# Performance work log

Measured on AMD Instinct MI355X. Metric: run time of the kernel, lower is better.

The kernel has to match this reference:

```python
import jax, jax.numpy as jnp
import numpy as np


def conv1x1(x, W, b):
    # 1x1 Conv2d == per-pixel linear over channels. x: [B,C,H,W], W: [O,C], b: [O]
    return jnp.einsum('oc,bchw->bohw', W, x) + b[None, :, None, None]


def setup_inputs() -> dict:
    key = jax.random.key(0)
    ks = jax.random.split(key, 18)
    B, C, Hd, H, W = 16, 64, 64, 32, 32
    s = 0.05
    f = jax.random.normal
    return {
        'h': f(ks[0], (B, C, H, W), jnp.float32),
        'm': f(ks[1], (B, C, H, W), jnp.float32),
        'Wq': f(ks[2], (Hd, C), jnp.float32) * s,
        'bq': f(ks[3], (Hd,), jnp.float32) * s,
        'Wk': f(ks[4], (Hd, C), jnp.float32) * s,
        'bk': f(ks[5], (Hd,), jnp.float32) * s,
        'Wk2': f(ks[6], (Hd, C), jnp.float32) * s,
        'bk2': f(ks[7], (Hd,), jnp.float32) * s,
        'Wv': f(ks[8], (C, C), jnp.float32) * s,
        'bv': f(ks[9], (C,), jnp.float32) * s,
        'Wv2': f(ks[10], (C, C), jnp.float32) * s,
        'bv2': f(ks[11], (C,), jnp.float32) * s,
        'Wz': f(ks[12], (2 * C, 2 * C), jnp.float32) * s,
        'bz': f(ks[13], (2 * C,), jnp.float32) * s,
        'Wm': f(ks[14], (3 * C, 3 * C), jnp.float32) * s,
        'bm': f(ks[15], (3 * C,), jnp.float32) * s,
    }


def reference(h, m, Wq, bq, Wk, bk, Wk2, bk2, Wv, bv, Wv2, bv2, Wz, bz, Wm, bm):
    B, C, H, W = h.shape
    Hd = Wq.shape[0]
    N = H * W
    # Shared query from h
    Q_h = conv1x1(h, Wq, bq).reshape(B, Hd, N).transpose(0, 2, 1)  # [B,N,Hd]
    # Self-attention branch over h
    K_h = conv1x1(h, Wk, bk).reshape(B, Hd, N)                     # [B,Hd,N]
    A_h = jax.nn.softmax(jnp.einsum('bnd,bdm->bnm', Q_h, K_h), axis=-1)  # [B,N,N]
    V_h = conv1x1(h, Wv, bv).reshape(B, C, N)                      # [B,C,N]
    Z_h = jnp.einsum('bnm,bcm->bcn', A_h, V_h).reshape(B, C, H, W)
    # Cross-attention branch over memory m (same query Q_h)
    K_m = conv1x1(m, Wk2, bk2).reshape(B, Hd, N)
    A_m = jax.nn.softmax(jnp.einsum('bnd,bdm->bnm', Q_h, K_m), axis=-1)
    V_m = conv1x1(m, Wv2, bv2).reshape(B, C, N)
    Z_m = jnp.einsum('bnm,bcm->bcn', A_m, V_m).reshape(B, C, H, W)
    # Fuse and gated memory update
    Z = conv1x1(jnp.concatenate([Z_h, Z_m], axis=1), Wz, bz)       # [B,2C,H,W]
    combined = conv1x1(jnp.concatenate([Z, h], axis=1), Wm, bm)    # [B,3C,H,W]
    mo, mg, mi = combined[:, :C], combined[:, C:2 * C], combined[:, 2 * C:]
    mi = jax.nn.sigmoid(mi)
    new_m = (1 - mi) * m + mi * jnp.tanh(mg)
    new_h = jax.nn.sigmoid(mo) * new_m
    return (new_h, new_m)
```

## Files before the change

### kernel.cpp

```cpp
#include <hip/hip_runtime.h>

typedef unsigned short u16;
typedef unsigned int u32;
typedef __attribute__((ext_vector_type(8))) short bf16x8;
typedef __attribute__((ext_vector_type(4))) short bf16x4;
typedef __attribute__((ext_vector_type(4))) float f32x4;

#define MFMA(a, b, c) __builtin_amdgcn_mfma_f32_16x16x32_bf16((a), (b), (c), 0, 0, 0)
#define MFMA16(a, b, c) __builtin_amdgcn_mfma_f32_16x16x16bf16_1k((a), (b), (c), 0, 0, 0)

static __device__ __forceinline__ u16 f2bf(float x) {
  u32 u = __float_as_uint(x);
  u += 0x7FFFu + ((u >> 16) & 1u);
  return (u16)(u >> 16);
}
static __device__ __forceinline__ u32 packbf_t(float hi, float lo) {
  return __builtin_amdgcn_perm(__float_as_uint(hi), __float_as_uint(lo), 0x07060302u);
}
static __device__ __forceinline__ u32 packbf(float lo, float hi) {
  return (u32)f2bf(lo) | ((u32)f2bf(hi) << 16);
}

__global__ __launch_bounds__(256) void proj_kernel(
    const float* __restrict__ h, const float* __restrict__ m_,
    const float* __restrict__ bq, const float* __restrict__ bk,
    const float* __restrict__ bk2, const float* __restrict__ bv,
    const float* __restrict__ bv2,
    const float* __restrict__ Wq, const float* __restrict__ Wk,
    const float* __restrict__ Wk2, const float* __restrict__ Wv,
    const float* __restrict__ Wv2,
    const float* __restrict__ Wz, const float* __restrict__ Wm,
    const float* __restrict__ bm,
    u16* __restrict__ Qb, u16* __restrict__ Khb, u16* __restrict__ Kmb,
    u16* __restrict__ Vhb, u16* __restrict__ Vmb, u16* __restrict__ hbuf,
    u16* __restrict__ Wzb, u16* __restrict__ Wmb, float* __restrict__ bmp)
{
  const int tid = threadIdx.x;
  const int b = blockIdx.y, n0 = blockIdx.x * 64, z = blockIdx.z;

  {
    const int gid = (blockIdx.z * 256 + blockIdx.y * 16 + blockIdx.x) * 256 + tid;
    if (gid < 16384) {
      Wzb[gid] = f2bf(Wz[gid]);
    } else if (gid < 53248) {
      const int e = gid - 16384;
      const int p = e / 192, k = e % 192;
      const int hb2 = p / 96, r1 = p % 96, ctl = r1 / 48, r2 = r1 % 48;
      const int g = r2 >> 4, mm = r2 & 15;
      const int o = g * 64 + (hb2 * 2 + ctl) * 16 + mm;
      Wmb[p * 192 + k] = f2bf(Wm[o * 192 + k]);
    } else if (gid < 53440) {
      const int p = gid - 53248;
      const int hb2 = p / 96, r1 = p % 96, ctl = r1 / 48, r2 = r1 % 48;
      const int g = r2 >> 4, mm = r2 & 15;
      const int o = g * 64 + (hb2 * 2 + ctl) * 16 + mm;
      bmp[p] = bm[o];
    }
  }

  __shared__ __align__(16) u16 xt[64][72];
  const float* __restrict__ X = (z >= 3) ? m_ : h;

  {
    const int px = tid & 63, c0 = (tid >> 6) * 16;
#pragma unroll
    for (int i = 0; i < 8; ++i) {
      const int c = c0 + 2 * i;
      const float f0 = X[(b * 64 + c) * 1024 + n0 + px];
      const float f1 = X[(b * 64 + c + 1) * 1024 + n0 + px];
      *(u32*)&xt[px][c] = packbf(f0, f1);
    }
  }
  __syncthreads();

  const int lane = tid & 63, w = tid >> 6;
  const int mm = lane & 15, q = lane >> 4;

  const bf16x8 xa0 = *(const bf16x8*)&xt[w * 16 + mm][q * 8];
  const bf16x8 xa1 = *(const bf16x8*)&xt[w * 16 + mm][32 + q * 8];

  auto ldw8 = [&](const float* Wf, int row, int col0) {
    const float4 a = *(const float4*)(Wf + row * 64 + col0);
    const float4 bb = *(const float4*)(Wf + row * 64 + col0 + 4);
    union { u32 u[4]; bf16x8 v; } r;
    r.u[0] = packbf(a.x, a.y);
    r.u[1] = packbf(a.z, a.w);
    r.u[2] = packbf(bb.x, bb.y);
    r.u[3] = packbf(bb.z, bb.w);
    return r.v;
  };

  auto qk_store = [&](u16* dst, const float* Wf, const float* bias) {
#pragma unroll
    for (int ot = 0; ot < 4; ++ot) {
      const bf16x8 wb0 = ldw8(Wf, ot * 16 + mm, q * 8);
      const bf16x8 wb1 = ldw8(Wf, ot * 16 + mm, 32 + q * 8);
      const float4 b4 = *(const float4*)(bias + ot * 16 + q * 4);
      f32x4 d = {b4.x, b4.y, b4.z, b4.w};
      d = MFMA(wb0, xa0, d);
      d = MFMA(wb1, xa1, d);
      uint2 val;
      val.x = packbf(d[0], d[1]);
      val.y = packbf(d[2], d[3]);
      *(uint2*)(dst + (b * 1024 + n0 + w * 16 + mm) * 64 + ot * 16 + q * 4) = val;
    }
  };
  auto v_store = [&](u16* dst, const float* Wf, const float* bias) {
#pragma unroll
    for (int ot = 0; ot < 4; ++ot) {
      const bf16x8 wb0 = ldw8(Wf, ot * 16 + mm, q * 8);
      const bf16x8 wb1 = ldw8(Wf, ot * 16 + mm, 32 + q * 8);
      const float bb = bias[ot * 16 + mm];
      f32x4 d = {bb, bb, bb, bb};
      d = MFMA(xa0, wb0, d);
      d = MFMA(xa1, wb1, d);
      uint2 val;
      val.x = packbf(d[0], d[1]);
      val.y = packbf(d[2], d[3]);
      *(uint2*)(dst + b * 65536 + blockIdx.x * 4096 + w * 1024 +
                (ot * 16 + mm) * 16 + q * 4) = val;
    }
  };

  if (z == 0) {
    qk_store(Qb, Wq, bq);
    const int px = tid >> 2, sg = tid & 3;
    u32* dst = (u32*)(hbuf + (b * 1024 + n0 + px) * 64 + sg * 16);
    const u16* srcr = &xt[px][sg * 16];
#pragma unroll
    for (int j = 0; j < 8; ++j) dst[j] = *(const u32*)(srcr + 2 * j);
  } else if (z == 1) {
    qk_store(Khb, Wk, bk);
  } else if (z == 2) {
    v_store(Vhb, Wv, bv);
  } else if (z == 3) {
    qk_store(Kmb, Wk2, bk2);
  } else {
    v_store(Vmb, Wv2, bv2);
  }
}

__global__ __launch_bounds__(256) void attn_kernel(
    const u16* __restrict__ Qb, const u16* __restrict__ Khb,
    const u16* __restrict__ Kmb, const u16* __restrict__ Vhb,
    const u16* __restrict__ Vmb, u16* __restrict__ Ztb)
{
  const int id = blockIdx.x;
  const int b = id & 15;
  const int br = (id >> 4) & 1;
  const int qh = id >> 5;
  const u16* __restrict__ K = (br ? Kmb : Khb) + b * 65536;
  const u16* __restrict__ V = (br ? Vmb : Vhb) + b * 65536;

  __shared__ __align__(16) u16 pool[21504];
  __shared__ float rsw[4][64];

  const int tid = threadIdx.x, w = tid >> 6, lane = tid & 63;
  const int mm = lane & 15, q = lane >> 4;
  const int q0 = qh * 64;

  u16* const warena = pool + w * 5376;

  bf16x8 qb0[4], qb1[4];
#pragma unroll
  for (int qt = 0; qt < 4; ++qt) {
    const u16* Qp = Qb + (b * 1024 + q0 + qt * 16 + mm) * 64;
    qb0[qt] = *(const bf16x8*)(Qp + q * 8);
    qb1[qt] = *(const bf16x8*)(Qp + 32 + q * 8);
  }

  f32x4 z[4][4];
#pragma unroll
  for (int qt = 0; qt < 4; ++qt)
#pragma unroll
    for (int ct = 0; ct < 4; ++ct) z[qt][ct] = (f32x4){0.f, 0.f, 0.f, 0.f};
  float rp[4] = {0.f, 0.f, 0.f, 0.f};

  uint4 k0, k1, v0, v1;
  auto ldg = [&](int kc) {
    const u16* Ks = K + kc * 4096 + w * 1024 + lane * 16;
    const u16* Vs = V + kc * 4096 + w * 1024 + lane * 16;
    k0 = *(const uint4*)Ks;
    k1 = *(const uint4*)(Ks + 8);
    v0 = *(const uint4*)Vs;
    v1 = *(const uint4*)(Vs + 8);
  };
  auto stl = [&](int buf) {
    u16* Kd = warena + buf * 2688 + (lane >> 2) * 72 + (lane & 3) * 16;
    u16* Vd = warena + buf * 2688 + 1152 + lane * 24;
    *(uint4*)Kd = k0;
    *(uint4*)(Kd + 8) = k1;
    *(uint4*)Vd = v0;
    *(uint4*)(Vd + 8) = v1;
  };

  auto compute = [&](int buf) {
    const u16* Kt = warena + buf * 2688;
    const u16* Vt = warena + buf * 2688 + 1152;
    const bf16x8 kf0 = *(const bf16x8*)(Kt + mm * 72 + q * 8);
    const bf16x8 kf1 = *(const bf16x8*)(Kt + mm * 72 + 32 + q * 8);
    bf16x4 vf[4];
#pragma unroll
    for (int ct = 0; ct < 4; ++ct)
      vf[ct] = *(const bf16x4*)(Vt + (ct * 16 + mm) * 24 + q * 4);

#pragma unroll
    for (int qt = 0; qt < 4; ++qt) {
      f32x4 s = {0.f, 0.f, 0.f, 0.f};
      s = MFMA(kf0, qb0[qt], s);
      s = MFMA(kf1, qb1[qt], s);
      const float e0 = __expf(s[0]), e1 = __expf(s[1]);
      const float e2 = __expf(s[2]), e3 = __expf(s[3]);
      rp[qt] += (e0 + e1) + (e2 + e3);
      union { u32 u[2]; bf16x4 v; } pb;
      pb.u[0] = packbf_t(e1, e0);
      pb.u[1] = packbf_t(e3, e2);
#pragma unroll
      for (int ct = 0; ct < 4; ++ct) z[qt][ct] = MFMA16(vf[ct], pb.v, z[qt][ct]);
    }
  };

  ldg(0);
  stl(0);
  ldg(1);

  int cur = 0;
#pragma unroll 1
  for (int kc = 0; kc < 16; ++kc) {
    compute(cur);
    if (kc < 15) {
      stl(cur ^ 1);
      if (kc < 14) ldg(kc + 2);
      cur ^= 1;
    }
  }

  __syncthreads();

  u16* const zcb = pool;
#pragma unroll
  for (int qt = 0; qt < 4; ++qt) {
    float v = rp[qt];
    v += __shfl_xor(v, 16);
    v += __shfl_xor(v, 32);
    if (q == 0) rsw[w][qt * 16 + mm] = v;
#pragma unroll
    for (int ct = 0; ct < 4; ++ct) {
      uint2 val;
      val.x = packbf_t(z[qt][ct][1], z[qt][ct][0]);
      val.y = packbf_t(z[qt][ct][3], z[qt][ct][2]);
      *(uint2*)(zcb + w * 4352 + (qt * 16 + mm) * 68 + ct * 16 + q * 4) = val;
    }
  }
  __syncthreads();

  const int c2 = tid & 31, qr = tid >> 5;
#pragma unroll
  for (int i = 0; i < 8; ++i) {
    const int query = qr + i * 8;
    const float rt = rsw[0][query] + rsw[1][query] + rsw[2][query] + rsw[3][query];
    const float rinv = __builtin_amdgcn_rcpf(rt);
    float vlo = 0.f, vhi = 0.f;
#pragma unroll
    for (int ww = 0; ww < 4; ++ww) {
      const u32 u = *(const u32*)(zcb + ww * 4352 + query * 68 + c2 * 2);
      vlo += __uint_as_float(u << 16);
      vhi += __uint_as_float(u & 0xffff0000u);
    }
    vlo *= rinv;
    vhi *= rinv;
    *(u32*)(Ztb + (b * 1024 + q0 + query) * 128 + br * 64 + c2 * 2) = packbf_t(vhi, vlo);
  }
}

__global__ __launch_bounds__(256) void tail_kernel(
    const u16* __restrict__ Ztb, const u16* __restrict__ hbuf,
    const float* __restrict__ m_, const u16* __restrict__ Wzb,
    const float* __restrict__ bz, const u16* __restrict__ Wmb,
    const float* __restrict__ bmp, float* __restrict__ out)
{
  const int b = blockIdx.y, n0 = blockIdx.x * 16;
  __shared__ __align__(16) u16 zp[16][136];
  const int tid = threadIdx.x, lane = tid & 63, wv = tid >> 6;
  const int mm = lane & 15, q = lane >> 4;

  {
    bf16x8 za[4];
#pragma unroll
    for (int ks = 0; ks < 4; ++ks)
      za[ks] = *(const bf16x8*)(Ztb + (b * 1024 + n0 + mm) * 128 + ks * 32 + q * 8);
#pragma unroll
    for (int ot = 0; ot < 2; ++ot) {
      const int o0 = wv * 32 + ot * 16;
      const float4 b4 = *(const float4*)(bz + o0 + q * 4);
      f32x4 d = {b4.x, b4.y, b4.z, b4.w};
#pragma unroll
      for (int ks = 0; ks < 4; ++ks) {
        const bf16x8 wb = *(const bf16x8*)(Wzb + (o0 + mm) * 128 + ks * 32 + q * 8);
        d = MFMA(wb, za[ks], d);
      }
      uint2 val;
      val.x = packbf(d[0], d[1]);
      val.y = packbf(d[2], d[3]);
      *(uint2*)&zp[mm][o0 + q * 4] = val;
    }
  }
  __syncthreads();

  {
    bf16x8 fa[6];
#pragma unroll
    for (int ks = 0; ks < 4; ++ks)
      fa[ks] = *(const bf16x8*)&zp[mm][ks * 32 + q * 8];
    {
      const u16* hp = hbuf + (b * 1024 + n0 + mm) * 64;
      fa[4] = *(const bf16x8*)(hp + q * 8);
      fa[5] = *(const bf16x8*)(hp + 32 + q * 8);
    }
    f32x4 dd[3];
#pragma unroll
    for (int j = 0; j < 3; ++j) {
      const int p = wv * 48 + j * 16 + mm;
      const float bb = bmp[p];
      f32x4 d = {bb, bb, bb, bb};
#pragma unroll
      for (int ks = 0; ks < 6; ++ks) {
        const bf16x8 wb = *(const bf16x8*)(Wmb + p * 192 + ks * 32 + q * 8);
        d = MFMA(fa[ks], wb, d);
      }
      dd[j] = d;
    }
    const int c = wv * 16 + mm;
    const int px = n0 + q * 4;
    const float4 mold = *(const float4*)(m_ + (b * 64 + c) * 1024 + px);
    float4 nh, nm;
#pragma unroll
    for (int r = 0; r < 4; ++r) {
      const float xo = dd[0][r];
      const float xg = dd[1][r];
      const float xi = dd[2][r];
      const float si = __builtin_amdgcn_rcpf(1.f + __expf(-xi));
      const float th = 1.f - 2.f * __builtin_amdgcn_rcpf(__expf(2.f * xg) + 1.f);
      const float so = __builtin_amdgcn_rcpf(1.f + __expf(-xo));
      const float mo = ((const float*)&mold)[r];
      const float nmv = (1.f - si) * mo + si * th;
      ((float*)&nm)[r] = nmv;
      ((float*)&nh)[r] = so * nmv;
    }
    *(float4*)(out + (b * 64 + c) * 1024 + px) = nh;
    *(float4*)(out + 1048576 + (b * 64 + c) * 1024 + px) = nm;
  }
}

extern "C" void kernel_launch(void* const* d_in, const int* in_sizes, int n_in,
                              void* d_out, int out_size, void* d_ws, size_t ws_size,
                              hipStream_t stream) {
  const float* h   = (const float*)d_in[0];
  const float* m   = (const float*)d_in[1];
  const float* Wq  = (const float*)d_in[2];
  const float* bq  = (const float*)d_in[3];
  const float* Wk  = (const float*)d_in[4];
  const float* bk  = (const float*)d_in[5];
  const float* Wk2 = (const float*)d_in[6];
  const float* bk2 = (const float*)d_in[7];
  const float* Wv  = (const float*)d_in[8];
  const float* bv  = (const float*)d_in[9];
  const float* Wv2 = (const float*)d_in[10];
  const float* bv2 = (const float*)d_in[11];
  const float* Wz  = (const float*)d_in[12];
  const float* bz  = (const float*)d_in[13];
  const float* Wm  = (const float*)d_in[14];
  const float* bm  = (const float*)d_in[15];
  float* out = (float*)d_out;

  char* ws = (char*)d_ws;
  const size_t MB = 1024 * 1024;
  u16* Qb   = (u16*)(ws + 0 * MB);
  u16* Khb  = (u16*)(ws + 2 * MB);
  u16* Kmb  = (u16*)(ws + 4 * MB);
  u16* Vhb  = (u16*)(ws + 6 * MB);
  u16* Vmb  = (u16*)(ws + 8 * MB);
  u16* hbuf = (u16*)(ws + 10 * MB);
  u16* Ztb  = (u16*)(ws + 12 * MB);
  u16* Wzb  = (u16*)(ws + 16 * MB + 40960);
  u16* Wmb  = (u16*)(ws + 16 * MB + 73728);
  float* bmp = (float*)(ws + 16 * MB + 147456);

  proj_kernel<<<dim3(16, 16, 5), 256, 0, stream>>>(
      h, m, bq, bk, bk2, bv, bv2, Wq, Wk, Wk2, Wv, Wv2, Wz, Wm, bm,
      Qb, Khb, Kmb, Vhb, Vmb, hbuf, Wzb, Wmb, bmp);
  attn_kernel<<<512, 256, 0, stream>>>(Qb, Khb, Kmb, Vhb, Vmb, Ztb);
  tail_kernel<<<dim3(64, 16), 256, 0, stream>>>(Ztb, hbuf, m, Wzb, bz, Wmb, bmp, out);
}
```

Baseline: 138.7 us.

## Fuse attention and tail kernels, each block handling both branches for 32 queries

Merges the attention kernel and the output tail kernel into one launch. Each block now processes 32 queries and runs both the self and cross attention passes in sequence, then applies the Wz and Wm projections and the gating from shared memory. This removes the Ztb global round-trip and one kernel launch. In exchange, each block re-reads K/V for both branches with half the query reuse, so each block does twice the serial attention work per query tile.

```diff
diff --git a/kernel.cpp b/kernel.cpp
--- a/kernel.cpp
+++ b/kernel.cpp
@@ -140,44 +140,53 @@
   }
 }
 
-__global__ __launch_bounds__(256) void attn_kernel(
+__global__ __launch_bounds__(256) void attn_tail_kernel(
     const u16* __restrict__ Qb, const u16* __restrict__ Khb,
     const u16* __restrict__ Kmb, const u16* __restrict__ Vhb,
-    const u16* __restrict__ Vmb, u16* __restrict__ Ztb)
+    const u16* __restrict__ Vmb, const u16* __restrict__ hbuf,
+    const float* __restrict__ m_, const u16* __restrict__ Wzb,
+    const float* __restrict__ bz, const u16* __restrict__ Wmb,
+    const float* __restrict__ bmp, float* __restrict__ out)
 {
   const int id = blockIdx.x;
   const int b = id & 15;
-  const int br = (id >> 4) & 1;
-  const int qh = id >> 5;
-  const u16* __restrict__ K = (br ? Kmb : Khb) + b * 65536;
-  const u16* __restrict__ V = (br ? Vmb : Vhb) + b * 65536;
+  const int qg = id >> 4;
+  const int q0 = qg * 32;
+
+  const u16* __restrict__ Kh = Khb + b * 65536;
+  const u16* __restrict__ Vh = Vhb + b * 65536;
+  const u16* __restrict__ Km = Kmb + b * 65536;
+  const u16* __restrict__ Vm = Vmb + b * 65536;
 
   __shared__ __align__(16) u16 pool[21504];
-  __shared__ float rsw[4][64];
+  __shared__ __align__(16) u16 zp[32][136];
+  __shared__ float rsw[4][32];
 
   const int tid = threadIdx.x, w = tid >> 6, lane = tid & 63;
   const int mm = lane & 15, q = lane >> 4;
-  const int q0 = qh * 64;
 
   u16* const warena = pool + w * 5376;
 
-  bf16x8 qb0[4], qb1[4];
-#pragma unroll
-  for (int qt = 0; qt < 4; ++qt) {
+  bf16x8 qb0[2], qb1[2];
+#pragma unroll
+  for (int qt = 0; qt < 2; ++qt) {
     const u16* Qp = Qb + (b * 1024 + q0 + qt * 16 + mm) * 64;
     qb0[qt] = *(const bf16x8*)(Qp + q * 8);
     qb1[qt] = *(const bf16x8*)(Qp + 32 + q * 8);
   }
 
-  f32x4 z[4][4];
-#pragma unroll
-  for (int qt = 0; qt < 4; ++qt)
-#pragma unroll
-    for (int ct = 0; ct < 4; ++ct) z[qt][ct] = (f32x4){0.f, 0.f, 0.f, 0.f};
-  float rp[4] = {0.f, 0.f, 0.f, 0.f};
+  f32x4 zA[2][4], zB[2][4];
+  float rpA[2] = {0.f, 0.f}, rpB[2] = {0.f, 0.f};
+#pragma unroll
+  for (int qt = 0; qt < 2; ++qt)
+#pragma unroll
+    for (int ct = 0; ct < 4; ++ct) {
+      zA[qt][ct] = (f32x4){0.f, 0.f, 0.f, 0.f};
+      zB[qt][ct] = (f32x4){0.f, 0.f, 0.f, 0.f};
+    }
 
   uint4 k0, k1, v0, v1;
-  auto ldg = [&](int kc) {
+  auto ldg = [&](const u16* K, const u16* V, int kc) {
     const u16* Ks = K + kc * 4096 + w * 1024 + lane * 16;
     const u16* Vs = V + kc * 4096 + w * 1024 + lane * 16;
     k0 = *(const uint4*)Ks;
@@ -194,7 +203,7 @@
     *(uint4*)(Vd + 8) = v1;
   };
 
-  auto compute = [&](int buf) {
+  auto compute = [&](int buf, f32x4 (&z)[2][4], float (&rp)[2]) {
     const u16* Kt = warena + buf * 2688;
     const u16* Vt = warena + buf * 2688 + 1152;
     const bf16x8 kf0 = *(const bf16x8*)(Kt + mm * 72 + q * 8);
@@ -205,7 +214,7 @@
       vf[ct] = *(const bf16x4*)(Vt + (ct * 16 + mm) * 24 + q * 4);
 
 #pragma unroll
-    for (int qt = 0; qt < 4; ++qt) {
+    for (int qt = 0; qt < 2; ++qt) {
       f32x4 s = {0.f, 0.f, 0.f, 0.f};
       s = MFMA(kf0, qb0[qt], s);
       s = MFMA(kf1, qb1[qt], s);
@@ -220,78 +229,77 @@
     }
   };
 
-  ldg(0);
-  stl(0);
-  ldg(1);
-
-  int cur = 0;
+  auto attn_pass = [&](const u16* K, const u16* V, f32x4 (&z)[2][4],
+                       float (&rp)[2]) {
+    ldg(K, V, 0);
+    stl(0);
+    ldg(K, V, 1);
+    int cur = 0;
 #pragma unroll 1
-  for (int kc = 0; kc < 16; ++kc) {
-    compute(cur);
-    if (kc < 15) {
-      stl(cur ^ 1);
-      if (kc < 14) ldg(kc + 2);
-      cur ^= 1;
-    }
-  }
+    for (int kc = 0; kc < 16; ++kc) {
+      compute(cur, z, rp);
+      if (kc < 15) {
+        stl(cur ^ 1);
+        if (kc < 14) ldg(K, V, kc + 2);
+        cur ^= 1;
+      }
+    }
+  };
+
+  attn_pass(Kh, Vh, zA, rpA);
+  attn_pass(Km, Vm, zB, rpB);
 
   __syncthreads();
 
   u16* const zcb = pool;
-#pragma unroll
-  for (int qt = 0; qt < 4; ++qt) {
-    float v = rp[qt];
-    v += __shfl_xor(v, 16);
-    v += __shfl_xor(v, 32);
-    if (q == 0) rsw[w][qt * 16 + mm] = v;
-#pragma unroll
-    for (int ct = 0; ct < 4; ++ct) {
-      uint2 val;
-      val.x = packbf_t(z[qt][ct][1], z[qt][ct][0]);
-      val.y = packbf_t(z[qt][ct][3], z[qt][ct][2]);
-      *(uint2*)(zcb + w * 4352 + (qt * 16 + mm) * 68 + ct * 16 + q * 4) = val;
-    }
-  }
-  __syncthreads();
-
-  const int c2 = tid & 31, qr = tid >> 5;
-#pragma unroll
-  for (int i = 0; i < 8; ++i) {
-    const int query = qr + i * 8;
-    const float rt = rsw[0][query] + rsw[1][query] + rsw[2][query] + rsw[3][query];
-    const float rinv = __builtin_amdgcn_rcpf(rt);
-    float vlo = 0.f, vhi = 0.f;
-#pragma unroll
-    for (int ww = 0; ww < 4; ++ww) {
-      const u32 u = *(const u32*)(zcb + ww * 4352 + query * 68 + c2 * 2);
-      vlo += __uint_as_float(u << 16);
-      vhi += __uint_as_float(u & 0xffff0000u);
-    }
-    vlo *= rinv;
-    vhi *= rinv;
-    *(u32*)(Ztb + (b * 1024 + q0 + query) * 128 + br * 64 + c2 * 2) = packbf_t(vhi, vlo);
-  }
-}
-
-__global__ __launch_bounds__(256) void tail_kernel(
-    const u16* __restrict__ Ztb, const u16* __restrict__ hbuf,
-    const float* __restrict__ m_, const u16* __restrict__ Wzb,
-    const float* __restrict__ bz, const u16* __restrict__ Wmb,
-    const float* __restrict__ bmp, float* __restrict__ out)
-{
-  const int b = blockIdx.y, n0 = blockIdx.x * 16;
-  __shared__ __align__(16) u16 zp[16][136];
-  const int tid = threadIdx.x, lane = tid & 63, wv = tid >> 6;
-  const int mm = lane & 15, q = lane >> 4;
-
+  auto combine = [&](int br, f32x4 (&z)[2][4], float (&rp)[2]) {
+#pragma unroll
+    for (int qt = 0; qt < 2; ++qt) {
+      float v = rp[qt];
+      v += __shfl_xor(v, 16);
+      v += __shfl_xor(v, 32);
+      if (q == 0) rsw[w][qt * 16 + mm] = v;
+#pragma unroll
+      for (int ct = 0; ct < 4; ++ct) {
+        uint2 val;
+        val.x = packbf_t(z[qt][ct][1], z[qt][ct][0]);
+        val.y = packbf_t(z[qt][ct][3], z[qt][ct][2]);
+        *(uint2*)(zcb + w * 2176 + (qt * 16 + mm) * 68 + ct * 16 + q * 4) = val;
+      }
+    }
+    __syncthreads();
+    const int c2 = tid & 31, qr = tid >> 5;
+#pragma unroll
+    for (int i = 0; i < 4; ++i) {
+      const int query = qr + i * 8;
+      const float rt = rsw[0][query] + rsw[1][query] + rsw[2][query] + rsw[3][query];
+      const float rinv = __builtin_amdgcn_rcpf(rt);
+      float vlo = 0.f, vhi = 0.f;
+#pragma unroll
+      for (int ww = 0; ww < 4; ++ww) {
+        const u32 u = *(const u32*)(zcb + ww * 2176 + query * 68 + c2 * 2);
+        vlo += __uint_as_float(u << 16);
+        vhi += __uint_as_float(u & 0xffff0000u);
+      }
+      vlo *= rinv;
+      vhi *= rinv;
+      *(u32*)&zp[query][br * 64 + c2 * 2] = packbf_t(vhi, vlo);
+    }
+    __syncthreads();
+  };
+  combine(0, zA, rpA);
+  combine(1, zB, rpB);
+
+  const int pxt = w & 1, oh = w >> 1;
+  u16* const zp2 = pool;
   {
     bf16x8 za[4];
 #pragma unroll
     for (int ks = 0; ks < 4; ++ks)
-      za[ks] = *(const bf16x8*)(Ztb + (b * 1024 + n0 + mm) * 128 + ks * 32 + q * 8);
-#pragma unroll
-    for (int ot = 0; ot < 2; ++ot) {
-      const int o0 = wv * 32 + ot * 16;
+      za[ks] = *(const bf16x8*)&zp[pxt * 16 + mm][ks * 32 + q * 8];
+#pragma unroll
+    for (int ot = 0; ot < 4; ++ot) {
+      const int o0 = oh * 64 + ot * 16;
       const float4 b4 = *(const float4*)(bz + o0 + q * 4);
       f32x4 d = {b4.x, b4.y, b4.z, b4.w};
 #pragma unroll
@@ -302,25 +310,26 @@
       uint2 val;
       val.x = packbf(d[0], d[1]);
       val.y = packbf(d[2], d[3]);
-      *(uint2*)&zp[mm][o0 + q * 4] = val;
+      *(uint2*)(zp2 + (pxt * 16 + mm) * 136 + o0 + q * 4) = val;
     }
   }
   __syncthreads();
 
   {
+    const int hb2 = oh;
     bf16x8 fa[6];
 #pragma unroll
     for (int ks = 0; ks < 4; ++ks)
-      fa[ks] = *(const bf16x8*)&zp[mm][ks * 32 + q * 8];
+      fa[ks] = *(const bf16x8*)(zp2 + (pxt * 16 + mm) * 136 + ks * 32 + q * 8);
     {
-      const u16* hp = hbuf + (b * 1024 + n0 + mm) * 64;
+      const u16* hp = hbuf + (b * 1024 + q0 + pxt * 16 + mm) * 64;
       fa[4] = *(const bf16x8*)(hp + q * 8);
       fa[5] = *(const bf16x8*)(hp + 32 + q * 8);
     }
-    f32x4 dd[3];
-#pragma unroll
-    for (int j = 0; j < 3; ++j) {
-      const int p = wv * 48 + j * 16 + mm;
+    f32x4 dd[6];
+#pragma unroll
+    for (int j = 0; j < 6; ++j) {
+      const int p = hb2 * 96 + j * 16 + mm;
       const float bb = bmp[p];
       f32x4 d = {bb, bb, bb, bb};
 #pragma unroll
@@ -330,25 +339,28 @@
       }
       dd[j] = d;
     }
-    const int c = wv * 16 + mm;
-    const int px = n0 + q * 4;
-    const float4 mold = *(const float4*)(m_ + (b * 64 + c) * 1024 + px);
-    float4 nh, nm;
-#pragma unroll
-    for (int r = 0; r < 4; ++r) {
-      const float xo = dd[0][r];
-      const float xg = dd[1][r];
-      const float xi = dd[2][r];
-      const float si = __builtin_amdgcn_rcpf(1.f + __expf(-xi));
-      const float th = 1.f - 2.f * __builtin_amdgcn_rcpf(__expf(2.f * xg) + 1.f);
-      const float so = __builtin_amdgcn_rcpf(1.f + __expf(-xo));
-      const float mo = ((const float*)&mold)[r];
-      const float nmv = (1.f - si) * mo + si * th;
-      ((float*)&nm)[r] = nmv;
-      ((float*)&nh)[r] = so * nmv;
-    }
-    *(float4*)(out + (b * 64 + c) * 1024 + px) = nh;
-    *(float4*)(out + 1048576 + (b * 64 + c) * 1024 + px) = nm;
+#pragma unroll
+    for (int ctl = 0; ctl < 2; ++ctl) {
+      const int c = (hb2 * 2 + ctl) * 16 + mm;
+      const int px = q0 + pxt * 16 + q * 4;
+      const float4 mold = *(const float4*)(m_ + (b * 64 + c) * 1024 + px);
+      float4 nh, nm;
+#pragma unroll
+      for (int r = 0; r < 4; ++r) {
+        const float xo = dd[ctl * 3 + 0][r];
+        const float xg = dd[ctl * 3 + 1][r];
+        const float xi = dd[ctl * 3 + 2][r];
+        const float si = __builtin_amdgcn_rcpf(1.f + __expf(-xi));
+        const float th = 1.f - 2.f * __builtin_amdgcn_rcpf(__expf(2.f * xg) + 1.f);
+        const float so = __builtin_amdgcn_rcpf(1.f + __expf(-xo));
+        const float mo = ((const float*)&mold)[r];
+        const float nmv = (1.f - si) * mo + si * th;
+        ((float*)&nm)[r] = nmv;
+        ((float*)&nh)[r] = so * nmv;
+      }
+      *(float4*)(out + (b * 64 + c) * 1024 + px) = nh;
+      *(float4*)(out + 1048576 + (b * 64 + c) * 1024 + px) = nm;
+    }
   }
 }
 
@@ -381,7 +393,6 @@
   u16* Vhb  = (u16*)(ws + 6 * MB);
   u16* Vmb  = (u16*)(ws + 8 * MB);
   u16* hbuf = (u16*)(ws + 10 * MB);
-  u16* Ztb  = (u16*)(ws + 12 * MB);
   u16* Wzb  = (u16*)(ws + 16 * MB + 40960);
   u16* Wmb  = (u16*)(ws + 16 * MB + 73728);
   float* bmp = (float*)(ws + 16 * MB + 147456);
@@ -389,6 +400,6 @@
   proj_kernel<<<dim3(16, 16, 5), 256, 0, stream>>>(
       h, m, bq, bk, bk2, bv, bv2, Wq, Wk, Wk2, Wv, Wv2, Wz, Wm, bm,
       Qb, Khb, Kmb, Vhb, Vmb, hbuf, Wzb, Wmb, bmp);
-  attn_kernel<<<512, 256, 0, stream>>>(Qb, Khb, Kmb, Vhb, Vmb, Ztb);
-  tail_kernel<<<dim3(64, 16), 256, 0, stream>>>(Ztb, hbuf, m, Wzb, bz, Wmb, bmp, out);
-}
+  attn_tail_kernel<<<512, 256, 0, stream>>>(Qb, Khb, Kmb, Vhb, Vmb, hbuf, m,
+                                            Wzb, bz, Wmb, bmp, out);
+}
```

New measurement: 138.5 us. About the same (-0.2%).
